# Optimization experiments

Measured on AMD Instinct MI355X. Metric: run time of the kernel, lower is better.

The kernel has to match this reference:

```python
import jax, jax.numpy as jnp
import numpy as np

B = 1024
IN_SHAPE = ((8, 8, 8), (8, 8))
IN_RANKS = ((32, 32, 32), (32, 32))
OUT_SHAPE = (16, 16, 16)
OUT_RANK = (32, 32, 32)


def _xavier(key, shape):
    # xavier_normal over axes [0,1] (in) and [2] (out), matching the torch helper
    fan_in = shape[0] * shape[1]
    fan_out = shape[2]
    std = float(np.sqrt(2.0 / (fan_in + fan_out)))
    return jax.random.normal(key, shape, dtype=jnp.float32) * std


def setup_inputs() -> dict:
    key = jax.random.key(0)
    ks = jax.random.split(key, 12)
    x_dims = tuple(d for g in IN_SHAPE for d in g)
    inp = {"x": jax.random.normal(ks[0], (B,) + x_dims, dtype=jnp.float32)}
    # input TT factors, flattened over groups in order (group, mode)
    fac_shapes = []
    for shapes, ranks in zip(IN_SHAPE, IN_RANKS):
        for i in range(len(shapes)):
            r_prev = 1 if i == 0 else ranks[i - 1]
            fac_shapes.append((r_prev, shapes[i], ranks[i]))
    for idx, fs in enumerate(fac_shapes):
        inp[f"f{idx}"] = _xavier(ks[1 + idx], fs)
    # core: (last rank of each group..., output_rank[-1])
    core_shape = tuple(r[-1] for r in IN_RANKS) + (OUT_RANK[-1],)
    fan_in = int(np.prod(core_shape[:-1]))
    std = float(np.sqrt(2.0 / (fan_in + core_shape[-1])))
    inp["core"] = jax.random.normal(ks[6], core_shape, dtype=jnp.float32) * std
    # output TT factors
    for i in range(len(OUT_SHAPE)):
        r_prev = 1 if i == 0 else OUT_RANK[i - 1]
        inp[f"g{i}"] = _xavier(ks[7 + i], (r_prev, OUT_SHAPE[i], OUT_RANK[i]))
    # bias: uniform(-1/sqrt(fan_in), +) with fan_in = total input features
    total_in = int(np.prod([np.prod(s) for s in IN_SHAPE]))
    bound = 1.0 / float(np.sqrt(total_in))
    inp["bias"] = jax.random.uniform(ks[10], OUT_SHAPE, dtype=jnp.float32,
                                     minval=-bound, maxval=bound)
    return inp


def reference(x, f0, f1, f2, f3, f4, core, g0, g1, g2, bias):
    groups = ((f0, f1, f2), (f3, f4))
    Bsz = x.shape[0]
    # T: [B, remaining_modes_flat, accumulated_group_ranks_flat]
    T = x.reshape(Bsz, -1)[:, :, None]
    for facs in groups:
        first = facs[0][0]                       # squeeze dummy rank-1: [n, r]
        n = first.shape[0]
        T = T.reshape(Bsz, n, -1, T.shape[-1])   # [B, n, M', Racc]
        T = jnp.einsum("bnmq,nr->bmqr", T, first)  # [B, M', Racc, r]
        for f in facs[1:]:
            n = f.shape[1]
            T = T.reshape(Bsz, n, -1, T.shape[-2], T.shape[-1])
            T = jnp.einsum("bnmqp,pnr->bmqr", T, f)
        # fold this group's final rank into the accumulated rank axis
        T = T.reshape(Bsz, T.shape[1], -1)
    # all input modes consumed -> T is [B, 1, r1_last*r2_last]
    z = T.reshape(Bsz, -1) @ core.reshape(-1, core.shape[-1])  # [B, Rout]
    # output TT chain -> W[o0, o1, o2, R_last]
    W = g0[0]
    for g in (g1, g2):
        W = jnp.einsum("...p,poq->...oq", W, g)
    R = W.shape[-1]
    out = z @ W.reshape(-1, R).T                 # [B, prod(OUT_SHAPE)]
    out = out.reshape((Bsz,) + OUT_SHAPE)
    return out + bias
```

## Files before the change

kernel.cpp:

```cpp
#include <hip/hip_runtime.h>
#include <stdint.h>

#define WS_M2 0
#define WS_N2 16384
#define WS_WT 18432
#define WS_Z  149504

#define GLOAD_LDS16(gsrc, ldst)                                         \
    __builtin_amdgcn_global_load_lds(                                   \
        (const __attribute__((address_space(1))) uint32_t*)(gsrc),      \
        (__attribute__((address_space(3))) uint32_t*)(ldst), 16, 0, 0)

#define FMA4(A, X, mm) do { (A).x += (X).x*(mm); (A).y += (X).y*(mm); \
                            (A).z += (X).z*(mm); (A).w += (X).w*(mm); } while (0)

__global__ __launch_bounds__(256) void precompute_kernel(
    const float* __restrict__ f0, const float* __restrict__ f1,
    const float* __restrict__ f2, const float* __restrict__ f3,
    const float* __restrict__ f4, const float* __restrict__ g0,
    const float* __restrict__ g1, const float* __restrict__ g2,
    float* __restrict__ ws)
{
    __shared__ float sA[8192];
    const int t = threadIdx.x;
    const int blk = blockIdx.x;
    if (blk < 8) {
        for (int i = t; i < 2048; i += 256) {
            int a01 = i >> 5, r2 = i & 31;
            int a0 = a01 >> 3, a1 = a01 & 7;
            float s = 0.f;
            #pragma unroll
            for (int r1 = 0; r1 < 32; ++r1)
                s += f0[a0*32 + r1] * f1[r1*256 + a1*32 + r2];
            sA[i] = s;
        }
        __syncthreads();
        for (int i = t; i < 2048; i += 256) {
            int a012 = blk*64 + (i >> 5), r3 = i & 31;
            int a01 = a012 >> 3, a2 = a012 & 7;
            float s = 0.f;
            #pragma unroll
            for (int r2 = 0; r2 < 32; ++r2)
                s += sA[a01*32 + r2] * f2[r2*256 + a2*32 + r3];
            ws[WS_M2 + a012*32 + r3] = s;
        }
    } else if (blk == 8) {
        for (int i = t; i < 2048; i += 256) {
            int a34 = i >> 5, s2 = i & 31;
            int a3 = a34 >> 3, a4 = a34 & 7;
            float s = 0.f;
            #pragma unroll
            for (int s1 = 0; s1 < 32; ++s1)
                s += f3[a3*32 + s1] * f4[s1*256 + a4*32 + s2];
            ws[WS_N2 + i] = s;
        }
    } else {
        const int j = blk - 9;
        for (int i = t; i < 8192; i += 256) {
            int o01 = i >> 5, q = i & 31;
            int o0 = o01 >> 4, o1 = o01 & 15;
            float s = 0.f;
            #pragma unroll
            for (int p = 0; p < 32; ++p)
                s += g0[o0*32 + p] * g1[p*512 + o1*32 + q];
            sA[i] = s;
        }
        __syncthreads();
        for (int i = t; i < 4096; i += 256) {
            int o = j*128 + (i >> 5);
            int r = i & 31;
            int o01 = o >> 4, o2 = o & 15;
            float s = 0.f;
            #pragma unroll
            for (int q = 0; q < 32; ++q)
                s += sA[o01*32 + q] * g2[q*512 + o2*32 + r];
            ws[WS_WT + r*4096 + o] = s;
        }
    }
}

__global__ __launch_bounds__(256, 3) void main_kernel(
    const float* __restrict__ x, const float* __restrict__ core,
    const float* __restrict__ ws, float* __restrict__ zout)
{
    __shared__ float s[12416];
    const int t = threadIdx.x;
    const int b = blockIdx.x;
    const int w    = __builtin_amdgcn_readfirstlane(t >> 6);
    const int lane = t & 63;
    const int tm = lane & 7;
    const int tr = lane >> 3;

    const float* __restrict__ xq  = x + (size_t)b*32768 + w*8192 + tm*8;
    const float* __restrict__ m2g = ws + WS_M2 + w*4096;
    float* __restrict__ mbuf = s + w*1024;

    GLOAD_LDS16(m2g + lane*4,       mbuf);
    GLOAD_LDS16(m2g + 256 + lane*4, mbuf + 256);
    asm volatile("s_waitcnt vmcnt(0)" ::: "memory");

    float4 accA[4], accB[4];
    #pragma unroll
    for (int rr = 0; rr < 4; ++rr) {
        accA[rr].x = accA[rr].y = accA[rr].z = accA[rr].w = 0.f;
        accB[rr].x = accB[rr].y = accB[rr].z = accB[rr].w = 0.f;
    }

    #pragma unroll 1
    for (int c = 0; c < 8; ++c) {
        if (c < 7) {
            const float* sm = m2g + (c+1)*512 + lane*4;
            float* dm = mbuf + ((c+1)&1)*512;
            GLOAD_LDS16(sm,       dm);
            GLOAD_LDS16(sm + 256, dm + 256);
        }
        const float* __restrict__ xc = xq + c*1024;
        const float* __restrict__ mc = mbuf + (c&1)*512 + tr*4;
        #pragma unroll 2
        for (int kk = 0; kk < 16; ++kk) {
            float4 xlo = *(const float4*)(xc + kk*64);
            float4 xhi = *(const float4*)(xc + kk*64 + 4);
            float4 m4  = *(const float4*)(mc + kk*32);
            FMA4(accA[0], xlo, m4.x); FMA4(accB[0], xhi, m4.x);
            FMA4(accA[1], xlo, m4.y); FMA4(accB[1], xhi, m4.y);
            FMA4(accA[2], xlo, m4.z); FMA4(accB[2], xhi, m4.z);
            FMA4(accA[3], xlo, m4.w); FMA4(accB[3], xhi, m4.w);
        }
        asm volatile("s_waitcnt vmcnt(0)" ::: "memory");
    }

    {
        float* pw = s + 4096 + w*2080;
        #pragma unroll
        for (int rr = 0; rr < 4; ++rr) {
            const int r = tr*4 + rr;
            float* d = pw + r*65 + tm*8;
            d[0]=accA[rr].x; d[1]=accA[rr].y; d[2]=accA[rr].z; d[3]=accA[rr].w;
            d[4]=accB[rr].x; d[5]=accB[rr].y; d[6]=accB[rr].z; d[7]=accB[rr].w;
        }
    }
    __syncthreads();

    {
        const float4* n24 = (const float4*)(ws + WS_N2);
        float4* d = (float4*)s;
        d[t]       = n24[t];
        d[256 + t] = n24[256 + t];
    }
    {
        float* P = s + 4096;
        const int rr  = t >> 3;
        const int mb2 = (t & 7) * 8;
        float sum[8];
        #pragma unroll
        for (int i = 0; i < 8; ++i) {
            sum[i] = P[rr*65 + mb2 + i] + P[2080 + rr*65 + mb2 + i]
                   + P[4160 + rr*65 + mb2 + i] + P[6240 + rr*65 + mb2 + i];
        }
        #pragma unroll
        for (int i = 0; i < 8; ++i) P[rr*65 + mb2 + i] = sum[i];
    }
    __syncthreads();

    {
        const float* P = s + 4096;
        const int r3  = t >> 3;
        const int s2b = (t & 7) * 4;
        float a0=0.f, a1=0.f, a2=0.f, a3=0.f;
        #pragma unroll 8
        for (int m = 0; m < 64; ++m) {
            float av = P[r3*65 + m];
            const float* n = &s[m*32 + s2b];
            a0 += av*n[0]; a1 += av*n[1]; a2 += av*n[2]; a3 += av*n[3];
        }
        float* d = &s[2048 + r3*32 + s2b];
        d[0]=a0; d[1]=a1; d[2]=a2; d[3]=a3;
    }
    __syncthreads();

    {
        const int ro2 = t & 15;
        const int kc  = t >> 4;
        const float2* core2 = (const float2*)core;
        float s0 = 0.f, s1 = 0.f;
        const int k0 = kc * 64;
        for (int k = k0; k < k0 + 64; ++k) {
            float tv = s[2048 + k];
            float2 cv = core2[k*16 + ro2];
            s0 += tv*cv.x; s1 += tv*cv.y;
        }
        s[3072 + kc*32 + ro2*2 + 0] = s0;
        s[3072 + kc*32 + ro2*2 + 1] = s1;
    }
    __syncthreads();
    if (t < 32) {
        float acc = 0.f;
        #pragma unroll
        for (int kc = 0; kc < 16; ++kc) acc += s[3072 + kc*32 + t];
        zout[b*32 + t] = acc;
    }
}

__global__ __launch_bounds__(256) void out_kernel(
    const float* __restrict__ ws, const float* __restrict__ bias,
    float* __restrict__ out)
{
    __shared__ float sW[8192];
    __shared__ float sZt[2176];
    __shared__ float sB[256];
    const int t  = threadIdx.x;
    const int bt = blockIdx.x;
    const int ot = blockIdx.y;

    {
        const float4* wt4 = (const float4*)(ws + WS_WT);
        float4* d = (float4*)sW;
        #pragma unroll
        for (int i = 0; i < 8; ++i) {
            int idx = i*256 + t;
            int ro = idx >> 6, oc = idx & 63;
            d[idx] = wt4[ro*1024 + ot*64 + oc];
        }
    }
    {
        const float4* z4 = (const float4*)(ws + WS_Z) + bt*512;
        #pragma unroll
        for (int i = 0; i < 2; ++i) {
            int idx = i*256 + t;
            int bl = idx >> 3, r4 = idx & 7;
            float4 v = z4[idx];
            sZt[(r4*4 + 0)*68 + bl] = v.x;
            sZt[(r4*4 + 1)*68 + bl] = v.y;
            sZt[(r4*4 + 2)*68 + bl] = v.z;
            sZt[(r4*4 + 3)*68 + bl] = v.w;
        }
    }
    if (t < 64) {
        const float4* b4 = (const float4*)bias + ot*64;
        ((float4*)sB)[t] = b4[t];
    }
    __syncthreads();

    const int oc = t & 63;
    const int bg = t >> 6;
    const float4* sW4 = (const float4*)sW;
    const float4 bv = ((const float4*)sB)[oc];
    float4* out4 = (float4*)out;

    for (int bi = 0; bi < 16; bi += 4) {
        const int bl = bg*16 + bi;
        float4 a0 = bv, a1 = bv, a2 = bv, a3 = bv;
        #pragma unroll
        for (int ro = 0; ro < 32; ++ro) {
            float4 w = sW4[ro*64 + oc];
            float4 z = *(const float4*)&sZt[ro*68 + bl];
            a0.x += z.x*w.x; a0.y += z.x*w.y; a0.z += z.x*w.z; a0.w += z.x*w.w;
            a1.x += z.y*w.x; a1.y += z.y*w.y; a1.z += z.y*w.z; a1.w += z.y*w.w;
            a2.x += z.z*w.x; a2.y += z.z*w.y; a2.z += z.z*w.z; a2.w += z.z*w.w;
            a3.x += z.w*w.x; a3.y += z.w*w.y; a3.z += z.w*w.z; a3.w += z.w*w.w;
        }
        const size_t obase = (size_t)(bt*64 + bl) * 1024 + ot*64 + oc;
        out4[obase + 0*1024] = a0;
        out4[obase + 1*1024] = a1;
        out4[obase + 2*1024] = a2;
        out4[obase + 3*1024] = a3;
    }
}

extern "C" void kernel_launch(void* const* d_in, const int* in_sizes, int n_in,
                              void* d_out, int out_size, void* d_ws, size_t ws_size,
                              hipStream_t stream)
{
    const float* x    = (const float*)d_in[0];
    const float* f0   = (const float*)d_in[1];
    const float* f1   = (const float*)d_in[2];
    const float* f2   = (const float*)d_in[3];
    const float* f3   = (const float*)d_in[4];
    const float* f4   = (const float*)d_in[5];
    const float* core = (const float*)d_in[6];
    const float* g0   = (const float*)d_in[7];
    const float* g1   = (const float*)d_in[8];
    const float* g2   = (const float*)d_in[9];
    const float* bias = (const float*)d_in[10];
    float* ws  = (float*)d_ws;
    float* out = (float*)d_out;

    precompute_kernel<<<41, 256, 0, stream>>>(f0, f1, f2, f3, f4, g0, g1, g2, ws);
    main_kernel<<<1024, 256, 0, stream>>>(x, core, ws, ws + WS_Z);
    out_kernel<<<dim3(16, 16), 256, 0, stream>>>(ws, bias, out);
}
```

Baseline: 314.2 us.

## Stage x tiles through LDS with async loads and swizzled partials

Each wave now streams its slice of x into LDS with global_load_lds in double-buffered chunks, alongside the M2 factor, instead of reading x straight from global memory into registers. The N2 factor load is folded into the last iteration, and the cross-wave partial sums use an XOR-swizzled layout instead of padded rows. Together these shrink LDS use so the launch bound can rise from 3 to 4 blocks per CU. In exchange it adds more wait points and LDS traffic for the x data.

After: 265.2 us. 15.6% less time.

```diff
diff --git a/kernel.cpp b/kernel.cpp
--- a/kernel.cpp
+++ b/kernel.cpp
@@ -79,11 +79,11 @@
     }
 }
 
-__global__ __launch_bounds__(256, 3) void main_kernel(
+__global__ __launch_bounds__(256, 4) void main_kernel(
     const float* __restrict__ x, const float* __restrict__ core,
     const float* __restrict__ ws, float* __restrict__ zout)
 {
-    __shared__ float s[12416];
+    __shared__ float s[10240];
     const int t = threadIdx.x;
     const int b = blockIdx.x;
     const int w    = __builtin_amdgcn_readfirstlane(t >> 6);
@@ -91,13 +91,13 @@
     const int tm = lane & 7;
     const int tr = lane >> 3;
 
-    const float* __restrict__ xq  = x + (size_t)b*32768 + w*8192 + tm*8;
-    const float* __restrict__ m2g = ws + WS_M2 + w*4096;
-    float* __restrict__ mbuf = s + w*1024;
-
-    GLOAD_LDS16(m2g + lane*4,       mbuf);
-    GLOAD_LDS16(m2g + 256 + lane*4, mbuf + 256);
-    asm volatile("s_waitcnt vmcnt(0)" ::: "memory");
+    float* __restrict__ R = s + w*2048;
+    const float* __restrict__ xg = x + (size_t)b*32768 + w*8192;
+    const float* __restrict__ mg = ws + WS_M2 + w*4096;
+
+    GLOAD_LDS16(xg + lane*4,        R);
+    GLOAD_LDS16(xg + 256 + lane*4,  R + 256);
+    GLOAD_LDS16(mg + lane*4,        R + 1024);
 
     float4 accA[4], accB[4];
     #pragma unroll
@@ -107,70 +107,65 @@
     }
 
     #pragma unroll 1
-    for (int c = 0; c < 8; ++c) {
-        if (c < 7) {
-            const float* sm = m2g + (c+1)*512 + lane*4;
-            float* dm = mbuf + ((c+1)&1)*512;
-            GLOAD_LDS16(sm,       dm);
-            GLOAD_LDS16(sm + 256, dm + 256);
-        }
-        const float* __restrict__ xc = xq + c*1024;
-        const float* __restrict__ mc = mbuf + (c&1)*512 + tr*4;
-        #pragma unroll 2
-        for (int kk = 0; kk < 16; ++kk) {
-            float4 xlo = *(const float4*)(xc + kk*64);
-            float4 xhi = *(const float4*)(xc + kk*64 + 4);
-            float4 m4  = *(const float4*)(mc + kk*32);
+    for (int c = 0; c < 16; ++c) {
+        if (c < 15) {
+            const float* sx = xg + (c+1)*512 + lane*4;
+            float* dx = R + ((c+1)&1)*512;
+            GLOAD_LDS16(sx,       dx);
+            GLOAD_LDS16(sx + 256, dx + 256);
+            GLOAD_LDS16(mg + (c+1)*256 + lane*4, R + 1024 + ((c+1)&1)*256);
+            asm volatile("s_waitcnt vmcnt(3)" ::: "memory");
+        } else {
+            const float* sn = ws + WS_N2 + w*512 + lane*4;
+            GLOAD_LDS16(sn,       s + 8192 + w*512);
+            GLOAD_LDS16(sn + 256, s + 8192 + w*512 + 256);
+            asm volatile("s_waitcnt vmcnt(2)" ::: "memory");
+        }
+        const float* __restrict__ xt = R + (c&1)*512 + tm*8;
+        const float* __restrict__ mt = R + 1024 + (c&1)*256 + tr*4;
+        #pragma unroll
+        for (int kk = 0; kk < 8; ++kk) {
+            float4 xlo = *(const float4*)(xt + kk*64);
+            float4 xhi = *(const float4*)(xt + kk*64 + 4);
+            float4 m4  = *(const float4*)(mt + kk*32);
             FMA4(accA[0], xlo, m4.x); FMA4(accB[0], xhi, m4.x);
             FMA4(accA[1], xlo, m4.y); FMA4(accB[1], xhi, m4.y);
             FMA4(accA[2], xlo, m4.z); FMA4(accB[2], xhi, m4.z);
             FMA4(accA[3], xlo, m4.w); FMA4(accB[3], xhi, m4.w);
         }
-        asm volatile("s_waitcnt vmcnt(0)" ::: "memory");
-    }
-
-    {
-        float* pw = s + 4096 + w*2080;
-        #pragma unroll
-        for (int rr = 0; rr < 4; ++rr) {
-            const int r = tr*4 + rr;
-            float* d = pw + r*65 + tm*8;
-            d[0]=accA[rr].x; d[1]=accA[rr].y; d[2]=accA[rr].z; d[3]=accA[rr].w;
-            d[4]=accB[rr].x; d[5]=accB[rr].y; d[6]=accB[rr].z; d[7]=accB[rr].w;
-        }
-    }
-    __syncthreads();
-
-    {
-        const float4* n24 = (const float4*)(ws + WS_N2);
-        float4* d = (float4*)s;
-        d[t]       = n24[t];
-        d[256 + t] = n24[256 + t];
-    }
-    {
-        float* P = s + 4096;
-        const int rr  = t >> 3;
-        const int mb2 = (t & 7) * 8;
-        float sum[8];
-        #pragma unroll
-        for (int i = 0; i < 8; ++i) {
-            sum[i] = P[rr*65 + mb2 + i] + P[2080 + rr*65 + mb2 + i]
-                   + P[4160 + rr*65 + mb2 + i] + P[6240 + rr*65 + mb2 + i];
-        }
-        #pragma unroll
-        for (int i = 0; i < 8; ++i) P[rr*65 + mb2 + i] = sum[i];
-    }
-    __syncthreads();
-
-    {
-        const float* P = s + 4096;
+    }
+
+    #pragma unroll
+    for (int rr = 0; rr < 4; ++rr) {
+        const int r = tr*4 + rr;
+        float* d = R + r*64 + ((tm ^ (r & 7)) << 3);
+        d[0]=accA[rr].x; d[1]=accA[rr].y; d[2]=accA[rr].z; d[3]=accA[rr].w;
+        d[4]=accB[rr].x; d[5]=accB[rr].y; d[6]=accB[rr].z; d[7]=accB[rr].w;
+    }
+    __syncthreads();
+
+    {
+        const int rr = t >> 3;
+        const int mo = t & 7;
+        const int off = rr*64 + (((mo ^ (rr & 7))) << 3);
+        float sm[8];
+        #pragma unroll
+        for (int i = 0; i < 8; ++i)
+            sm[i] = s[off + i] + s[2048 + off + i]
+                  + s[4096 + off + i] + s[6144 + off + i];
+        #pragma unroll
+        for (int i = 0; i < 8; ++i) s[off + i] = sm[i];
+    }
+    __syncthreads();
+
+    {
         const int r3  = t >> 3;
         const int s2b = (t & 7) * 4;
         float a0=0.f, a1=0.f, a2=0.f, a3=0.f;
         #pragma unroll 8
         for (int m = 0; m < 64; ++m) {
-            float av = P[r3*65 + m];
-            const float* n = &s[m*32 + s2b];
+            float av = s[r3*64 + (((m >> 3) ^ (r3 & 7)) << 3) + (m & 7)];
+            const float* n = &s[8192 + m*32 + s2b];
             a0 += av*n[0]; a1 += av*n[1]; a2 += av*n[2]; a3 += av*n[3];
         }
         float* d = &s[2048 + r3*32 + s2b];
```
